# Kernel optimization log

Hardware: AMD Instinct MI355X
Metric: run time of the kernel (lower is better)

The kernel has to match this reference:

```python
import jax, jax.numpy as jnp
import numpy as np

B, T, D, H = 4, 2048, 1024, 16
Dh = D // H  # 64


def setup_inputs() -> dict:
    key = jax.random.key(0)
    ks = jax.random.split(key, 12)
    s = 1.0 / np.sqrt(D)
    return {
        "q": jax.random.normal(ks[0], (B, T, D), jnp.float32),
        "k": jax.random.normal(ks[1], (B, T, D), jnp.float32),
        "v": jax.random.normal(ks[2], (B, T, D), jnp.float32),
        "Wq": jax.random.normal(ks[3], (D, D), jnp.float32) * s,
        "bq": jnp.zeros((D,), jnp.float32),
        "Wk": jax.random.normal(ks[4], (D, D), jnp.float32) * s,
        "bk": jnp.zeros((D,), jnp.float32),
        "Wv": jax.random.normal(ks[5], (Dh, D), jnp.float32) * s,
        "bv": jnp.zeros((Dh,), jnp.float32),
        "Wo": jax.random.normal(ks[6], (D, D), jnp.float32) * s,
        "bo": jnp.zeros((D,), jnp.float32),
    }


def reference(q, k, v, Wq, bq, Wk, bk, Wv, bv, Wo, bo):
    # Projections (torch Linear: y = x @ W.T + b)
    Q = (q @ Wq.T + bq).reshape(B, T, H, Dh)   # [B,T,H,Dh]
    K = (k @ Wk.T + bk).reshape(B, T, H, Dh)   # [B,T,H,Dh]
    Vs = v @ Wv.T + bv                         # [B,T,Dh] shared across heads
    scale = 1.0 / np.sqrt(Dh).astype(np.float32)
    scores = jnp.einsum('bqhd,bkhd->bhqk', Q, K) * scale  # [B,H,T,T]
    attn = jax.nn.softmax(scores, axis=-1)
    # shared-V: broadcast V over heads
    out = jnp.einsum('bhqk,bkd->bqhd', attn, Vs)  # [B,T,H,Dh]
    out = out.reshape(B, T, D)
    y = out @ Wo.T + bo                           # [B,T,D]
    return y, attn.mean(axis=1)                   # per-head-averaged attention
```

## Files before the change

kernel.cpp:

```cpp
#include <hip/hip_runtime.h>
#include <cstdint>
#include <cstddef>

typedef __attribute__((ext_vector_type(8))) _Float16 half8;
typedef __attribute__((ext_vector_type(4))) float f32x4;

#define DEV static __device__ __forceinline__

DEV half8 cvt8(const float* p) {
    f32x4 a = *(const f32x4*)p;
    f32x4 b = *(const f32x4*)(p + 4);
    half8 o;
    o[0] = (_Float16)a[0]; o[1] = (_Float16)a[1];
    o[2] = (_Float16)a[2]; o[3] = (_Float16)a[3];
    o[4] = (_Float16)b[0]; o[5] = (_Float16)b[1];
    o[6] = (_Float16)b[2]; o[7] = (_Float16)b[3];
    return o;
}

template<int BM, int BN, int WR, int WC, bool A_F16, bool OUT_F16, bool OUT_TRANS>
__global__ __launch_bounds__(256, 2)
void gemm_bt(const void* __restrict__ Aptr, const float* __restrict__ Bw,
             const float* __restrict__ bias, float scale,
             void* __restrict__ Cout, int M, int N, int K)
{
    constexpr int BK = 32;
    constexpr int WM = BM / WR, WN = BN / WC;
    constexpr int MF = WM / 16, NF = WN / 16;
    constexpr int LDT = 40;
    __shared__ _Float16 As[BM][LDT];
    __shared__ _Float16 Bs[BN][LDT];

    const int tid = threadIdx.x;
    const int l = tid & 63, w = tid >> 6;
    const int wr = w / WC, wc = w % WC;
    const int lr = l & 15, lh = l >> 4;
    const int bm0 = blockIdx.y * BM, bn0 = blockIdx.x * BN;

    f32x4 acc[MF][NF] = {};

    for (int k0 = 0; k0 < K; k0 += BK) {
        __syncthreads();
        for (int c = tid; c < BM * 4; c += 256) {
            int row = c >> 2, c8 = (c & 3) << 3;
            if constexpr (A_F16) {
                const _Float16* ap = (const _Float16*)Aptr + (size_t)(bm0 + row) * K + k0 + c8;
                *(half8*)&As[row][c8] = *(const half8*)ap;
            } else {
                const float* ap = (const float*)Aptr + (size_t)(bm0 + row) * K + k0 + c8;
                *(half8*)&As[row][c8] = cvt8(ap);
            }
        }
        for (int c = tid; c < BN * 4; c += 256) {
            int row = c >> 2, c8 = (c & 3) << 3;
            const float* bp = Bw + (size_t)(bn0 + row) * K + k0 + c8;
            *(half8*)&Bs[row][c8] = cvt8(bp);
        }
        __syncthreads();

        half8 a[MF], b[NF];
#pragma unroll
        for (int m = 0; m < MF; m++)
            a[m] = *(const half8*)&As[wr * WM + m * 16 + lr][lh * 8];
#pragma unroll
        for (int n = 0; n < NF; n++)
            b[n] = *(const half8*)&Bs[wc * WN + n * 16 + lr][lh * 8];
#pragma unroll
        for (int m = 0; m < MF; m++)
#pragma unroll
            for (int n = 0; n < NF; n++)
                acc[m][n] = __builtin_amdgcn_mfma_f32_16x16x32_f16(a[m], b[n], acc[m][n], 0, 0, 0);
    }

#pragma unroll
    for (int m = 0; m < MF; m++)
#pragma unroll
        for (int n = 0; n < NF; n++) {
            int row0 = bm0 + wr * WM + m * 16 + lh * 4;
            int col = bn0 + wc * WN + n * 16 + lr;
            float bv = bias[col];
#pragma unroll
            for (int j = 0; j < 4; j++) {
                float val = (acc[m][n][j] + bv) * scale;
                int row = row0 + j;
                if constexpr (OUT_TRANS) {
                    int bi = row >> 11, t = row & 2047;
                    ((_Float16*)Cout)[(((size_t)(bi * 64 + col)) << 11) + t] = (_Float16)val;
                } else if constexpr (OUT_F16) {
                    ((_Float16*)Cout)[(size_t)row * N + col] = (_Float16)val;
                } else {
                    ((float*)Cout)[(size_t)row * N + col] = val;
                }
            }
        }
}

__global__ __launch_bounds__(512, 2)
void attn_kernel(const _Float16* __restrict__ Qh, const _Float16* __restrict__ Kh,
                 const _Float16* __restrict__ VT, float* __restrict__ attn_out,
                 _Float16* __restrict__ Oh)
{
    const int blk = blockIdx.x;
    const int b = blk & 3;
    const int q0 = (blk >> 2) << 5;
    const int tid = threadIdx.x;
    const int l = tid & 63, w = tid >> 6;
    const int lr = l & 15, lh = l >> 4;
    const int h0 = w << 1;

    __shared__ float pw[8][32][33];
    __shared__ _Float16 Pld[8][32][40];

    const size_t base = (size_t)b * 2048 * 1024;
    const _Float16* Qb = Qh + base;
    const _Float16* Kb = Kh + base;

    half8 qf[2][2][2];
#pragma unroll
    for (int hh = 0; hh < 2; hh++)
#pragma unroll
        for (int m = 0; m < 2; m++)
#pragma unroll
            for (int dk = 0; dk < 2; dk++)
                qf[hh][m][dk] = *(const half8*)(Qb + (size_t)(q0 + m * 16 + lr) * 1024
                                                + (h0 + hh) * 64 + dk * 32 + lh * 8);

    float ml[2][2][4], sl[2][2][4];
#pragma unroll
    for (int hh = 0; hh < 2; hh++)
#pragma unroll
        for (int m = 0; m < 2; m++)
#pragma unroll
            for (int j = 0; j < 4; j++) { ml[hh][m][j] = -1e30f; sl[hh][m][j] = 0.f; }

    for (int kt = 0; kt < 64; kt++) {
        const _Float16* kp = Kb + (size_t)(kt * 32) * 1024;
#pragma unroll
        for (int hh = 0; hh < 2; hh++) {
            half8 kfh[2][2];
#pragma unroll
            for (int kfr = 0; kfr < 2; kfr++)
#pragma unroll
                for (int dk = 0; dk < 2; dk++)
                    kfh[kfr][dk] = *(const half8*)(kp + (size_t)(kfr * 16 + lr) * 1024
                                                   + (h0 + hh) * 64 + dk * 32 + lh * 8);
            f32x4 sc[2][2] = {};
#pragma unroll
            for (int m = 0; m < 2; m++)
#pragma unroll
                for (int kfr = 0; kfr < 2; kfr++)
#pragma unroll
                    for (int dk = 0; dk < 2; dk++)
                        sc[m][kfr] = __builtin_amdgcn_mfma_f32_16x16x32_f16(
                            qf[hh][m][dk], kfh[kfr][dk], sc[m][kfr], 0, 0, 0);
#pragma unroll
            for (int m = 0; m < 2; m++)
#pragma unroll
                for (int j = 0; j < 4; j++) {
                    float v0 = sc[m][0][j], v1 = sc[m][1][j];
                    float t = fmaxf(v0, v1);
                    float mo = ml[hh][m][j];
                    float mn = fmaxf(mo, t);
                    sl[hh][m][j] = sl[hh][m][j] * __builtin_amdgcn_exp2f(mo - mn)
                                 + __builtin_amdgcn_exp2f(v0 - mn)
                                 + __builtin_amdgcn_exp2f(v1 - mn);
                    ml[hh][m][j] = mn;
                }
        }
    }
#pragma unroll
    for (int hh = 0; hh < 2; hh++)
#pragma unroll
        for (int m = 0; m < 2; m++)
#pragma unroll
            for (int j = 0; j < 4; j++) {
                float mv = ml[hh][m][j], sv = sl[hh][m][j];
#pragma unroll
                for (int d = 1; d < 16; d <<= 1) {
                    float mo = __shfl_xor(mv, d, 64);
                    float so = __shfl_xor(sv, d, 64);
                    float mn = fmaxf(mv, mo);
                    sv = sv * __builtin_amdgcn_exp2f(mv - mn)
                       + so * __builtin_amdgcn_exp2f(mo - mn);
                    mv = mn;
                }
                ml[hh][m][j] = mv;
                sl[hh][m][j] = 1.0f / sv;
            }

    f32x4 oacc[2][2][4] = {};
    __syncthreads();

    for (int kt = 0; kt < 64; kt++) {
        const int krow = kt * 32;
        const _Float16* kp = Kb + (size_t)krow * 1024;
        half8 vf[4];
#pragma unroll
        for (int dv = 0; dv < 4; dv++)
            vf[dv] = *(const half8*)(VT + (((size_t)(b * 64 + dv * 16 + lr)) << 11) + krow + lh * 8);

        float psum[2][2][4] = {};
#pragma unroll
        for (int hh = 0; hh < 2; hh++) {
            half8 kfh[2][2];
#pragma unroll
            for (int kfr = 0; kfr < 2; kfr++)
#pragma unroll
                for (int dk = 0; dk < 2; dk++)
                    kfh[kfr][dk] = *(const half8*)(kp + (size_t)(kfr * 16 + lr) * 1024
                                                   + (h0 + hh) * 64 + dk * 32 + lh * 8);
            f32x4 sc[2][2] = {};
#pragma unroll
            for (int m = 0; m < 2; m++)
#pragma unroll
                for (int kfr = 0; kfr < 2; kfr++)
#pragma unroll
                    for (int dk = 0; dk < 2; dk++)
                        sc[m][kfr] = __builtin_amdgcn_mfma_f32_16x16x32_f16(
                            qf[hh][m][dk], kfh[kfr][dk], sc[m][kfr], 0, 0, 0);
#pragma unroll
            for (int m = 0; m < 2; m++)
#pragma unroll
                for (int kfr = 0; kfr < 2; kfr++)
#pragma unroll
                    for (int j = 0; j < 4; j++) {
                        float p = __builtin_amdgcn_exp2f(sc[m][kfr][j] - ml[hh][m][j]) * sl[hh][m][j];
                        psum[m][kfr][j] += p;
                        Pld[w][m * 16 + lh * 4 + j][kfr * 16 + lr] = (_Float16)p;
                    }
            half8 pa[2];
#pragma unroll
            for (int m = 0; m < 2; m++)
                pa[m] = *(const half8*)&Pld[w][m * 16 + lr][lh * 8];
#pragma unroll
            for (int m = 0; m < 2; m++)
#pragma unroll
                for (int dv = 0; dv < 4; dv++)
                    oacc[hh][m][dv] = __builtin_amdgcn_mfma_f32_16x16x32_f16(
                        pa[m], vf[dv], oacc[hh][m][dv], 0, 0, 0);
        }
#pragma unroll
        for (int m = 0; m < 2; m++)
#pragma unroll
            for (int kfr = 0; kfr < 2; kfr++)
#pragma unroll
                for (int j = 0; j < 4; j++)
                    pw[w][m * 16 + lh * 4 + j][kfr * 16 + lr] = psum[m][kfr][j];
        __syncthreads();
        for (int idx = tid; idx < 1024; idx += 512) {
            int r = idx >> 5, c = idx & 31;
            float s = 0.f;
#pragma unroll
            for (int ww = 0; ww < 8; ww++) s += pw[ww][r][c];
            attn_out[(((size_t)(b * 2048 + q0 + r)) << 11) + krow + c] = s * 0.0625f;
        }
        __syncthreads();
    }

#pragma unroll
    for (int hh = 0; hh < 2; hh++)
#pragma unroll
        for (int m = 0; m < 2; m++)
#pragma unroll
            for (int dv = 0; dv < 4; dv++)
#pragma unroll
                for (int j = 0; j < 4; j++) {
                    int row = q0 + m * 16 + lh * 4 + j;
                    int col = (h0 + hh) * 64 + dv * 16 + lr;
                    Oh[base + (size_t)row * 1024 + col] = (_Float16)oacc[hh][m][dv][j];
                }
}

extern "C" void kernel_launch(void* const* d_in, const int* in_sizes, int n_in,
                              void* d_out, int out_size, void* d_ws, size_t ws_size,
                              hipStream_t stream)
{
    const float* q  = (const float*)d_in[0];
    const float* k  = (const float*)d_in[1];
    const float* v  = (const float*)d_in[2];
    const float* Wq = (const float*)d_in[3];
    const float* bq = (const float*)d_in[4];
    const float* Wk = (const float*)d_in[5];
    const float* bk = (const float*)d_in[6];
    const float* Wv = (const float*)d_in[7];
    const float* bv = (const float*)d_in[8];
    const float* Wo = (const float*)d_in[9];
    const float* bo = (const float*)d_in[10];

    float* y = (float*)d_out;
    float* attn_mean = y + (size_t)4 * 2048 * 1024;

    uint8_t* ws = (uint8_t*)d_ws;
    _Float16* Qh = (_Float16*)(ws);
    _Float16* Kh = (_Float16*)(ws + (size_t)16 * 1024 * 1024);
    _Float16* VT = (_Float16*)(ws + (size_t)32 * 1024 * 1024);
    _Float16* Oh = (_Float16*)(ws + (size_t)34 * 1024 * 1024);

    const float QS = 0.125f * 1.44269504088896340736f;

    gemm_bt<128, 128, 2, 2, false, true, false><<<dim3(8, 64), dim3(256), 0, stream>>>(
        q, Wq, bq, QS, Qh, 8192, 1024, 1024);
    gemm_bt<128, 128, 2, 2, false, true, false><<<dim3(8, 64), dim3(256), 0, stream>>>(
        k, Wk, bk, 1.0f, Kh, 8192, 1024, 1024);
    gemm_bt<128, 64, 4, 1, false, true, true><<<dim3(1, 64), dim3(256), 0, stream>>>(
        v, Wv, bv, 1.0f, VT, 8192, 64, 1024);
    attn_kernel<<<dim3(256), dim3(512), 0, stream>>>(Qh, Kh, VT, attn_mean, Oh);
    gemm_bt<128, 128, 2, 2, true, false, false><<<dim3(8, 64), dim3(256), 0, stream>>>(
        Oh, Wo, bo, 1.0f, y, 8192, 1024, 1024);
}
```

Before: 631.7 us.

## Pre-convert to fp16, async double-buffered GEMM, split attention second pass

```diff
diff --git a/kernel.cpp b/kernel.cpp
--- a/kernel.cpp
+++ b/kernel.cpp
@@ -3,9 +3,12 @@
 #include <cstddef>
 
 typedef __attribute__((ext_vector_type(8))) _Float16 half8;
+typedef __attribute__((ext_vector_type(4))) _Float16 half4;
 typedef __attribute__((ext_vector_type(4))) float f32x4;
 
 #define DEV static __device__ __forceinline__
+#define AS1(p) (const __attribute__((address_space(1))) void*)(p)
+#define AS3(p) (__attribute__((address_space(3))) void*)(p)
 
 DEV half8 cvt8(const float* p) {
     f32x4 a = *(const f32x4*)p;
@@ -18,21 +21,114 @@
     return o;
 }
 
-template<int BM, int BN, int WR, int WC, bool A_F16, bool OUT_F16, bool OUT_TRANS>
+__global__ __launch_bounds__(256)
+void cvt_kernel(const float* __restrict__ in, _Float16* __restrict__ out, int n8)
+{
+    int i = blockIdx.x * 256 + threadIdx.x;
+    int stride = gridDim.x * 256;
+    for (; i < n8; i += stride)
+        ((half8*)out)[i] = cvt8(in + (size_t)i * 8);
+}
+
+__global__ __launch_bounds__(256)
+void opsum_kernel(const _Float16* __restrict__ a, const _Float16* __restrict__ b,
+                  _Float16* __restrict__ out, int n8)
+{
+    int i = blockIdx.x * 256 + threadIdx.x;
+    int stride = gridDim.x * 256;
+    for (; i < n8; i += stride) {
+        half8 x = ((const half8*)a)[i];
+        half8 y = ((const half8*)b)[i];
+        half8 o;
+#pragma unroll
+        for (int j = 0; j < 8; j++) o[j] = (_Float16)((float)x[j] + (float)y[j]);
+        ((half8*)out)[i] = o;
+    }
+}
+
+template<bool OUT_F16>
 __global__ __launch_bounds__(256, 2)
-void gemm_bt(const void* __restrict__ Aptr, const float* __restrict__ Bw,
-             const float* __restrict__ bias, float scale,
-             void* __restrict__ Cout, int M, int N, int K)
+void gemm16(const _Float16* __restrict__ A, const _Float16* __restrict__ B,
+            const float* __restrict__ bias, float scale, void* __restrict__ Cout,
+            int M, int N, int K)
+{
+    __shared__ half8 As[2][512];
+    __shared__ half8 Bs[2][512];
+    const int tid = threadIdx.x, l = tid & 63, w = tid >> 6;
+    const int lr = l & 15, lh = l >> 4;
+    const int wm0 = (w >> 1) * 64, wn0 = (w & 1) * 64;
+    const int bm0 = blockIdx.x * 128, bn0 = blockIdx.y * 128;
+    const int nsteps = K >> 5;
+
+    f32x4 acc[4][4] = {};
+
+#define STAGE(buf, t) do {                                                        \
+        int k0 = (t) << 5;                                                        \
+        _Pragma("unroll")                                                         \
+        for (int q2 = 0; q2 < 2; q2++) {                                          \
+            int r = q2 * 64 + l;                                                  \
+            __builtin_amdgcn_global_load_lds(                                     \
+                AS1(A + (size_t)(bm0 + r) * K + k0 + w * 8),                      \
+                AS3(&As[buf][w * 128 + q2 * 64]), 16, 0, 0);                      \
+            __builtin_amdgcn_global_load_lds(                                     \
+                AS1(B + (size_t)(bn0 + r) * K + k0 + w * 8),                      \
+                AS3(&Bs[buf][w * 128 + q2 * 64]), 16, 0, 0);                      \
+        }                                                                         \
+    } while (0)
+
+    STAGE(0, 0);
+    __syncthreads();
+    for (int t = 0; t < nsteps; t++) {
+        int cur = t & 1;
+        if (t + 1 < nsteps) STAGE(cur ^ 1, t + 1);
+        half8 a[4], b[4];
+#pragma unroll
+        for (int m = 0; m < 4; m++) a[m] = As[cur][lh * 128 + wm0 + m * 16 + lr];
+#pragma unroll
+        for (int n = 0; n < 4; n++) b[n] = Bs[cur][lh * 128 + wn0 + n * 16 + lr];
+#pragma unroll
+        for (int m = 0; m < 4; m++)
+#pragma unroll
+            for (int n = 0; n < 4; n++)
+                acc[m][n] = __builtin_amdgcn_mfma_f32_16x16x32_f16(a[m], b[n], acc[m][n], 0, 0, 0);
+        __syncthreads();
+    }
+#undef STAGE
+
+#pragma unroll
+    for (int m = 0; m < 4; m++)
+#pragma unroll
+        for (int n = 0; n < 4; n++) {
+            int row0 = bm0 + wm0 + m * 16 + lh * 4;
+            int col = bn0 + wn0 + n * 16 + lr;
+            float bv = bias[col];
+#pragma unroll
+            for (int j = 0; j < 4; j++) {
+                float val = (acc[m][n][j] + bv) * scale;
+                int row = row0 + j;
+                if constexpr (OUT_F16)
+                    ((_Float16*)Cout)[(size_t)row * N + col] = (_Float16)val;
+                else
+                    ((float*)Cout)[(size_t)row * N + col] = val;
+            }
+        }
+}
+
+template<int BM, int BN, int WR, int WC>
+__global__ __launch_bounds__(256, 2)
+void gemm_vp(const float* __restrict__ Aptr, const float* __restrict__ Bw,
+             const float* __restrict__ bias, _Float16* __restrict__ Cout, int M, int N, int K)
 {
     constexpr int BK = 32;
     constexpr int WM = BM / WR, WN = BN / WC;
     constexpr int MF = WM / 16, NF = WN / 16;
     constexpr int LDT = 40;
-    __shared__ _Float16 As[BM][LDT];
-    __shared__ _Float16 Bs[BN][LDT];
+    __shared__ _Float16 Asl[BM][LDT];
+    __shared__ _Float16 Bsl[BN][LDT];
 
     const int tid = threadIdx.x;
-    const int l = tid & 63, w = tid >> 6;
+    const int l = tid & 63;
+    const int w = tid >> 6;
     const int wr = w / WC, wc = w % WC;
     const int lr = l & 15, lh = l >> 4;
     const int bm0 = blockIdx.y * BM, bn0 = blockIdx.x * BN;
@@ -43,28 +139,21 @@
         __syncthreads();
         for (int c = tid; c < BM * 4; c += 256) {
             int row = c >> 2, c8 = (c & 3) << 3;
-            if constexpr (A_F16) {
-                const _Float16* ap = (const _Float16*)Aptr + (size_t)(bm0 + row) * K + k0 + c8;
-                *(half8*)&As[row][c8] = *(const half8*)ap;
-            } else {
-                const float* ap = (const float*)Aptr + (size_t)(bm0 + row) * K + k0 + c8;
-                *(half8*)&As[row][c8] = cvt8(ap);
-            }
+            *(half8*)&Asl[row][c8] = cvt8(Aptr + (size_t)(bm0 + row) * K + k0 + c8);
         }
         for (int c = tid; c < BN * 4; c += 256) {
             int row = c >> 2, c8 = (c & 3) << 3;
-            const float* bp = Bw + (size_t)(bn0 + row) * K + k0 + c8;
-            *(half8*)&Bs[row][c8] = cvt8(bp);
+            *(half8*)&Bsl[row][c8] = cvt8(Bw + (size_t)(bn0 + row) * K + k0 + c8);
         }
         __syncthreads();
 
         half8 a[MF], b[NF];
 #pragma unroll
         for (int m = 0; m < MF; m++)
-            a[m] = *(const half8*)&As[wr * WM + m * 16 + lr][lh * 8];
+            a[m] = *(const half8*)&Asl[wr * WM + m * 16 + lr][lh * 8];
 #pragma unroll
         for (int n = 0; n < NF; n++)
-            b[n] = *(const half8*)&Bs[wc * WN + n * 16 + lr][lh * 8];
+            b[n] = *(const half8*)&Bsl[wc * WN + n * 16 + lr][lh * 8];
 #pragma unroll
         for (int m = 0; m < MF; m++)
 #pragma unroll
@@ -81,35 +170,30 @@
             float bv = bias[col];
 #pragma unroll
             for (int j = 0; j < 4; j++) {
-                float val = (acc[m][n][j] + bv) * scale;
+                float val = acc[m][n][j] + bv;
                 int row = row0 + j;
-                if constexpr (OUT_TRANS) {
-                    int bi = row >> 11, t = row & 2047;
-                    ((_Float16*)Cout)[(((size_t)(bi * 64 + col)) << 11) + t] = (_Float16)val;
-                } else if constexpr (OUT_F16) {
-                    ((_Float16*)Cout)[(size_t)row * N + col] = (_Float16)val;
-                } else {
-                    ((float*)Cout)[(size_t)row * N + col] = val;
-                }
-            }
-        }
-}
-
-__global__ __launch_bounds__(512, 2)
+                int bi = row >> 11, t = row & 2047;
+                Cout[(((size_t)(bi * 64 + col)) << 11) + t] = (_Float16)val;
+            }
+        }
+}
+
+__global__ __launch_bounds__(512, 4)
 void attn_kernel(const _Float16* __restrict__ Qh, const _Float16* __restrict__ Kh,
                  const _Float16* __restrict__ VT, float* __restrict__ attn_out,
-                 _Float16* __restrict__ Oh)
+                 _Float16* __restrict__ Op)
 {
     const int blk = blockIdx.x;
     const int b = blk & 3;
-    const int q0 = (blk >> 2) << 5;
+    const int ks = (blk >> 2) & 1;
+    const int q0 = (blk >> 3) << 5;
     const int tid = threadIdx.x;
     const int l = tid & 63, w = tid >> 6;
     const int lr = l & 15, lh = l >> 4;
     const int h0 = w << 1;
 
-    __shared__ float pw[8][32][33];
-    __shared__ _Float16 Pld[8][32][40];
+    __shared__ float pw[8][32][34];
+    __shared__ _Float16 Pld[8][32][44];
 
     const size_t base = (size_t)b * 2048 * 1024;
     const _Float16* Qb = Qh + base;
@@ -125,16 +209,61 @@
                 qf[hh][m][dk] = *(const half8*)(Qb + (size_t)(q0 + m * 16 + lr) * 1024
                                                 + (h0 + hh) * 64 + dk * 32 + lh * 8);
 
-    float ml[2][2][4], sl[2][2][4];
-#pragma unroll
-    for (int hh = 0; hh < 2; hh++)
-#pragma unroll
-        for (int m = 0; m < 2; m++)
-#pragma unroll
-            for (int j = 0; j < 4; j++) { ml[hh][m][j] = -1e30f; sl[hh][m][j] = 0.f; }
-
+    float sl[2][2][4] = {};
     for (int kt = 0; kt < 64; kt++) {
         const _Float16* kp = Kb + (size_t)(kt * 32) * 1024;
+#pragma unroll
+        for (int hh = 0; hh < 2; hh++) {
+            half8 kfh[2][2];
+#pragma unroll
+            for (int kfr = 0; kfr < 2; kfr++)
+#pragma unroll
+                for (int dk = 0; dk < 2; dk++)
+                    kfh[kfr][dk] = *(const half8*)(kp + (size_t)(kfr * 16 + lr) * 1024
+                                                   + (h0 + hh) * 64 + dk * 32 + lh * 8);
+#pragma unroll
+            for (int m = 0; m < 2; m++) {
+                f32x4 sc[2] = {};
+#pragma unroll
+                for (int kfr = 0; kfr < 2; kfr++)
+#pragma unroll
+                    for (int dk = 0; dk < 2; dk++)
+                        sc[kfr] = __builtin_amdgcn_mfma_f32_16x16x32_f16(
+                            qf[hh][m][dk], kfh[kfr][dk], sc[kfr], 0, 0, 0);
+#pragma unroll
+                for (int j = 0; j < 4; j++)
+                    sl[hh][m][j] += __builtin_amdgcn_exp2f(sc[0][j])
+                                  + __builtin_amdgcn_exp2f(sc[1][j]);
+            }
+        }
+    }
+    float rinv[2][2][4];
+#pragma unroll
+    for (int hh = 0; hh < 2; hh++)
+#pragma unroll
+        for (int m = 0; m < 2; m++)
+#pragma unroll
+            for (int j = 0; j < 4; j++) {
+                float s = sl[hh][m][j];
+#pragma unroll
+                for (int d = 1; d < 16; d <<= 1)
+                    s += __shfl_xor(s, d, 64);
+                rinv[hh][m][j] = 1.0f / s;
+            }
+
+    f32x4 oacc[2][2][4] = {};
+    __syncthreads();
+
+    const int kt0 = ks * 32, kt1 = kt0 + 32;
+    for (int kt = kt0; kt < kt1; kt++) {
+        const int krow = kt * 32;
+        const _Float16* kp = Kb + (size_t)krow * 1024;
+        half8 vf[4];
+#pragma unroll
+        for (int dv = 0; dv < 4; dv++)
+            vf[dv] = *(const half8*)(VT + (((size_t)(b * 64 + dv * 16 + lr)) << 11) + krow + lh * 8);
+
+        float psum[2][2][4] = {};
 #pragma unroll
         for (int hh = 0; hh < 2; hh++) {
             half8 kfh[2][2];
@@ -156,88 +285,24 @@
 #pragma unroll
             for (int m = 0; m < 2; m++)
 #pragma unroll
-                for (int j = 0; j < 4; j++) {
-                    float v0 = sc[m][0][j], v1 = sc[m][1][j];
-                    float t = fmaxf(v0, v1);
-                    float mo = ml[hh][m][j];
-                    float mn = fmaxf(mo, t);
-                    sl[hh][m][j] = sl[hh][m][j] * __builtin_amdgcn_exp2f(mo - mn)
-                                 + __builtin_amdgcn_exp2f(v0 - mn)
-                                 + __builtin_amdgcn_exp2f(v1 - mn);
-                    ml[hh][m][j] = mn;
-                }
-        }
-    }
-#pragma unroll
-    for (int hh = 0; hh < 2; hh++)
-#pragma unroll
-        for (int m = 0; m < 2; m++)
-#pragma unroll
-            for (int j = 0; j < 4; j++) {
-                float mv = ml[hh][m][j], sv = sl[hh][m][j];
-#pragma unroll
-                for (int d = 1; d < 16; d <<= 1) {
-                    float mo = __shfl_xor(mv, d, 64);
-                    float so = __shfl_xor(sv, d, 64);
-                    float mn = fmaxf(mv, mo);
-                    sv = sv * __builtin_amdgcn_exp2f(mv - mn)
-                       + so * __builtin_amdgcn_exp2f(mo - mn);
-                    mv = mn;
-                }
-                ml[hh][m][j] = mv;
-                sl[hh][m][j] = 1.0f / sv;
-            }
-
-    f32x4 oacc[2][2][4] = {};
-    __syncthreads();
-
-    for (int kt = 0; kt < 64; kt++) {
-        const int krow = kt * 32;
-        const _Float16* kp = Kb + (size_t)krow * 1024;
-        half8 vf[4];
-#pragma unroll
-        for (int dv = 0; dv < 4; dv++)
-            vf[dv] = *(const half8*)(VT + (((size_t)(b * 64 + dv * 16 + lr)) << 11) + krow + lh * 8);
-
-        float psum[2][2][4] = {};
-#pragma unroll
-        for (int hh = 0; hh < 2; hh++) {
-            half8 kfh[2][2];
-#pragma unroll
-            for (int kfr = 0; kfr < 2; kfr++)
-#pragma unroll
-                for (int dk = 0; dk < 2; dk++)
-                    kfh[kfr][dk] = *(const half8*)(kp + (size_t)(kfr * 16 + lr) * 1024
-                                                   + (h0 + hh) * 64 + dk * 32 + lh * 8);
-            f32x4 sc[2][2] = {};
-#pragma unroll
-            for (int m = 0; m < 2; m++)
-#pragma unroll
                 for (int kfr = 0; kfr < 2; kfr++)
 #pragma unroll
-                    for (int dk = 0; dk < 2; dk++)
-                        sc[m][kfr] = __builtin_amdgcn_mfma_f32_16x16x32_f16(
-                            qf[hh][m][dk], kfh[kfr][dk], sc[m][kfr], 0, 0, 0);
-#pragma unroll
-            for (int m = 0; m < 2; m++)
-#pragma unroll
-                for (int kfr = 0; kfr < 2; kfr++)
-#pragma unroll
                     for (int j = 0; j < 4; j++) {
-                        float p = __builtin_amdgcn_exp2f(sc[m][kfr][j] - ml[hh][m][j]) * sl[hh][m][j];
+                        float p = __builtin_amdgcn_exp2f(sc[m][kfr][j]) * rinv[hh][m][j];
                         psum[m][kfr][j] += p;
                         Pld[w][m * 16 + lh * 4 + j][kfr * 16 + lr] = (_Float16)p;
                     }
-            half8 pa[2];
-#pragma unroll
-            for (int m = 0; m < 2; m++)
-                pa[m] = *(const half8*)&Pld[w][m * 16 + lr][lh * 8];
-#pragma unroll
-            for (int m = 0; m < 2; m++)
+#pragma unroll
+            for (int m = 0; m < 2; m++) {
+                union { half8 v8; half4 v4[2]; } pu;
+                pu.v4[0] = *(const half4*)&Pld[w][m * 16 + lr][lh * 8];
+                pu.v4[1] = *(const half4*)&Pld[w][m * 16 + lr][lh * 8 + 4];
+                half8 pa = pu.v8;
 #pragma unroll
                 for (int dv = 0; dv < 4; dv++)
                     oacc[hh][m][dv] = __builtin_amdgcn_mfma_f32_16x16x32_f16(
-                        pa[m], vf[dv], oacc[hh][m][dv], 0, 0, 0);
+                        pa, vf[dv], oacc[hh][m][dv], 0, 0, 0);
+            }
         }
 #pragma unroll
         for (int m = 0; m < 2; m++)
@@ -252,11 +317,13 @@
             float s = 0.f;
 #pragma unroll
             for (int ww = 0; ww < 8; ww++) s += pw[ww][r][c];
-            attn_out[(((size_t)(b * 2048 + q0 + r)) << 11) + krow + c] = s * 0.0625f;
-        }
-        __syncthreads();
-    }
-
+            __builtin_nontemporal_store(s * 0.0625f,
+                &attn_out[(((size_t)(b * 2048 + q0 + r)) << 11) + krow + c]);
+        }
+        __syncthreads();
+    }
+
+    _Float16* op = Op + (size_t)ks * 8388608 + base;
 #pragma unroll
     for (int hh = 0; hh < 2; hh++)
 #pragma unroll
@@ -267,7 +334,7 @@
                 for (int j = 0; j < 4; j++) {
                     int row = q0 + m * 16 + lh * 4 + j;
                     int col = (h0 + hh) * 64 + dv * 16 + lr;
-                    Oh[base + (size_t)row * 1024 + col] = (_Float16)oacc[hh][m][dv][j];
+                    op[(size_t)row * 1024 + col] = (_Float16)oacc[hh][m][dv][j];
                 }
 }
 
@@ -291,20 +358,31 @@
     float* attn_mean = y + (size_t)4 * 2048 * 1024;
 
     uint8_t* ws = (uint8_t*)d_ws;
-    _Float16* Qh = (_Float16*)(ws);
-    _Float16* Kh = (_Float16*)(ws + (size_t)16 * 1024 * 1024);
-    _Float16* VT = (_Float16*)(ws + (size_t)32 * 1024 * 1024);
-    _Float16* Oh = (_Float16*)(ws + (size_t)34 * 1024 * 1024);
+    _Float16* Qh  = (_Float16*)(ws);
+    _Float16* Kh  = (_Float16*)(ws + 16777216);
+    _Float16* VT  = (_Float16*)(ws + 33554432);
+    _Float16* Wqc = (_Float16*)(ws + 34603008);
+    _Float16* Wkc = (_Float16*)(ws + 36700160);
+    _Float16* Woc = (_Float16*)(ws + 38797312);
+    _Float16* qc  = (_Float16*)(ws + 40894464);
+    _Float16* kc  = (_Float16*)(ws + 57671680);
+    _Float16* Op  = qc;
 
     const float QS = 0.125f * 1.44269504088896340736f;
 
-    gemm_bt<128, 128, 2, 2, false, true, false><<<dim3(8, 64), dim3(256), 0, stream>>>(
-        q, Wq, bq, QS, Qh, 8192, 1024, 1024);
-    gemm_bt<128, 128, 2, 2, false, true, false><<<dim3(8, 64), dim3(256), 0, stream>>>(
-        k, Wk, bk, 1.0f, Kh, 8192, 1024, 1024);
-    gemm_bt<128, 64, 4, 1, false, true, true><<<dim3(1, 64), dim3(256), 0, stream>>>(
-        v, Wv, bv, 1.0f, VT, 8192, 64, 1024);
-    attn_kernel<<<dim3(256), dim3(512), 0, stream>>>(Qh, Kh, VT, attn_mean, Oh);
-    gemm_bt<128, 128, 2, 2, true, false, false><<<dim3(8, 64), dim3(256), 0, stream>>>(
-        Oh, Wo, bo, 1.0f, y, 8192, 1024, 1024);
-}
+    cvt_kernel<<<dim3(1024), dim3(256), 0, stream>>>(q, qc, 1048576);
+    cvt_kernel<<<dim3(1024), dim3(256), 0, stream>>>(k, kc, 1048576);
+    cvt_kernel<<<dim3(512),  dim3(256), 0, stream>>>(Wq, Wqc, 131072);
+    cvt_kernel<<<dim3(512),  dim3(256), 0, stream>>>(Wk, Wkc, 131072);
+    cvt_kernel<<<dim3(512),  dim3(256), 0, stream>>>(Wo, Woc, 131072);
+
+    gemm16<true><<<dim3(64, 8), dim3(256), 0, stream>>>(qc, Wqc, bq, QS, Qh, 8192, 1024, 1024);
+    gemm16<true><<<dim3(64, 8), dim3(256), 0, stream>>>(kc, Wkc, bk, 1.0f, Kh, 8192, 1024, 1024);
+    gemm_vp<128, 64, 4, 1><<<dim3(1, 64), dim3(256), 0, stream>>>(v, Wv, bv, VT, 8192, 64, 1024);
+
+    attn_kernel<<<dim3(512), dim3(512), 0, stream>>>(Qh, Kh, VT, attn_mean, Op);
+
+    opsum_kernel<<<dim3(1024), dim3(256), 0, stream>>>(Op, Op + (size_t)8388608, Op, 1048576);
+
+    gemm16<false><<<dim3(64, 8), dim3(256), 0, stream>>>(Op, Woc, bo, 1.0f, y, 8192, 1024, 1024);
+}
```

After: 982.5 us. 55.5% more time.
